# Kernel optimization log

Hardware: AMD Instinct MI355X
Metric: run time of the kernel (lower is better)

The kernel has to match this reference:

```python
import jax, jax.numpy as jnp
import numpy as np

NUM_Q_HEADS = 32
NUM_KV_HEADS = 8
GROUP = NUM_Q_HEADS // NUM_KV_HEADS  # 4, matches hardcoded repeat_interleave(repeats=4)
HEAD_DIM = 128
ROPE_BASE = 10000.0


def _rope_cos_sin(seq_len, head_dim, dtype):
    # [S, D/2] angle tables for rotate-half RoPE
    inv_freq = 1.0 / (ROPE_BASE ** (jnp.arange(0, head_dim, 2, dtype=jnp.float32) / head_dim))
    ang = jnp.arange(seq_len, dtype=jnp.float32)[:, None] * inv_freq[None, :]
    return jnp.cos(ang).astype(dtype), jnp.sin(ang).astype(dtype)


def _apply_rope(x, cos, sin):
    # x: [B, S, H, D]; cos/sin: [S, D/2] broadcast over batch & heads
    x1, x2 = jnp.split(x, 2, axis=-1)
    c = cos[None, :, None, :]
    s = sin[None, :, None, :]
    return jnp.concatenate([x1 * c - x2 * s, x2 * c + x1 * s], axis=-1)


def setup_inputs() -> dict:
    key = jax.random.key(0)
    k1, k2, k3 = jax.random.split(key, 3)
    B, S, E = 2, 2048, 4096
    x = jax.random.normal(k1, (B, S, E), dtype=jnp.float32)
    w_in = jax.random.normal(k2, (6144, E), dtype=jnp.float32) * 0.02   # torch Linear weight [out, in]
    w_out = jax.random.normal(k3, (E, E), dtype=jnp.float32) * 0.02
    return {"x": x, "w_in": w_in, "w_out": w_out}


def reference(x, w_in, w_out):
    B, S, E = x.shape
    D = HEAD_DIM
    qkv = jnp.einsum('bse,fe->bsf', x, w_in)  # [B, S, 6144]
    parts = jnp.split(qkv, GROUP + 2, axis=-1)  # 6 equal chunks of width E//GROUP
    q = jnp.concatenate(parts[:GROUP], axis=-1).reshape(B, S, NUM_Q_HEADS, D)
    k = parts[GROUP].reshape(B, S, NUM_KV_HEADS, D)
    v = parts[GROUP + 1].reshape(B, S, NUM_KV_HEADS, D)

    cos, sin = _rope_cos_sin(S, D, x.dtype)
    q = _apply_rope(q, cos, sin)
    k = _apply_rope(k, cos, sin)

    # GQA without materializing repeated K/V: group q heads by kv head.
    # repeat_interleave(k, 4, dim=2) maps q head h -> kv head h // 4, i.e. q view [B,S,HKV,G,D]
    qg = q.reshape(B, S, NUM_KV_HEADS, GROUP, D)
    scale = 1.0 / jnp.sqrt(jnp.asarray(D, dtype=x.dtype))
    scores = jnp.einsum('bqhgd,bkhd->bhgqk', qg, k) * scale  # [B, HKV, G, S, S]
    causal = jnp.tril(jnp.ones((S, S), dtype=bool))
    scores = jnp.where(causal[None, None, None, :, :], scores, jnp.asarray(-1e30, dtype=scores.dtype))
    probs = jax.nn.softmax(scores, axis=-1)
    out = jnp.einsum('bhgqk,bkhd->bqhgd', probs, v)  # [B, S, HKV, G, D]
    out = out.reshape(B, S, E)
    return jnp.einsum('bse,fe->bsf', out, w_out)
```

## Files before the change

### kernel.cpp

```cpp
#include <hip/hip_runtime.h>
#include <hip/hip_bf16.h>
#include <stdint.h>

typedef unsigned short u16;
typedef __bf16 bf16x8 __attribute__((ext_vector_type(8)));
typedef u16 u16x8 __attribute__((ext_vector_type(8)));
typedef float f32x4 __attribute__((ext_vector_type(4)));

#define DEV __device__ __forceinline__
#define SBAR() asm volatile("s_barrier" ::: "memory")

DEV u16 f2bf(float f) {
  uint32_t u = __builtin_bit_cast(uint32_t, f);
  return (u16)((u + 0x7FFFu + ((u >> 16) & 1u)) >> 16);
}
DEV float bf2f(u16 h) { return __builtin_bit_cast(float, (uint32_t)h << 16); }

DEV void gload_lds16(const void* g, void* l) {
  __builtin_amdgcn_global_load_lds((const __attribute__((address_space(1))) uint32_t*)g,
                                   (__attribute__((address_space(3))) uint32_t*)l, 16, 0, 0);
}

__global__ void cvt_bf16(const float* __restrict__ in, u16* __restrict__ out, int n) {
  int i = (blockIdx.x * 256 + threadIdx.x) * 8;
  if (i >= n) return;
  const float4* p = reinterpret_cast<const float4*>(in + i);
  float4 a = p[0], b = p[1];
  u16x8 o;
  o[0] = f2bf(a.x); o[1] = f2bf(a.y); o[2] = f2bf(a.z); o[3] = f2bf(a.w);
  o[4] = f2bf(b.x); o[5] = f2bf(b.y); o[6] = f2bf(b.z); o[7] = f2bf(b.w);
  *reinterpret_cast<u16x8*>(out + i) = o;
}

__global__ void rope_table(float* __restrict__ ct, float* __restrict__ st) {
  int i = blockIdx.x * 256 + threadIdx.x;
  int s = i >> 6, d = i & 63;
  float invf = powf(10000.0f, -(float)d * (1.0f / 64.0f));
  float ang = (float)s * invf;
  ct[i] = cosf(ang);
  st[i] = sinf(ang);
}

__global__ void rope_apply(u16* __restrict__ qkv, const float* __restrict__ ct, const float* __restrict__ st) {
  int idx = blockIdx.x * 256 + threadIdx.x;
  int grp = idx & 7;
  int head = (idx >> 3) % 40;
  int row = idx / 320;
  int s = row & 2047;
  size_t f0 = head < 32 ? (size_t)head * 128 : (size_t)4096 + (size_t)(head - 32) * 128;
  u16* p = qkv + (size_t)row * 6144 + f0 + grp * 8;
  u16x8 a = *reinterpret_cast<const u16x8*>(p);
  u16x8 b = *reinterpret_cast<const u16x8*>(p + 64);
  const float4* cp = reinterpret_cast<const float4*>(ct + s * 64 + grp * 8);
  const float4* sp = reinterpret_cast<const float4*>(st + s * 64 + grp * 8);
  float4 c0 = cp[0], c1 = cp[1], s0 = sp[0], s1 = sp[1];
  float cc[8] = {c0.x, c0.y, c0.z, c0.w, c1.x, c1.y, c1.z, c1.w};
  float ss[8] = {s0.x, s0.y, s0.z, s0.w, s1.x, s1.y, s1.z, s1.w};
  u16x8 o1, o2;
#pragma unroll
  for (int i = 0; i < 8; i++) {
    float x1 = bf2f(a[i]), x2 = bf2f(b[i]);
    o1[i] = f2bf(x1 * cc[i] - x2 * ss[i]);
    o2[i] = f2bf(x2 * cc[i] + x1 * ss[i]);
  }
  *reinterpret_cast<u16x8*>(p) = o1;
  *reinterpret_cast<u16x8*>(p + 64) = o2;
}

__global__ void prep_vt(const u16* __restrict__ qkv, u16* __restrict__ vtg) {
  int id = blockIdx.x;
  int j = id & 31, kvh = (id >> 5) & 7, b = id >> 8;
  const int tid = threadIdx.x;
  const size_t rowB = (size_t)b * 2048;
  u16* img = vtg + (size_t)id * 8192;
#pragma unroll
  for (int p = 0; p < 4; p++) {
    int lin = p * 256 + tid;
    int d = lin >> 3, c = lin & 7;
    const u16* src = qkv + (rowB + j * 64 + c * 8) * 6144 + 5120 + kvh * 128 + d;
    u16x8 v;
#pragma unroll
    for (int i = 0; i < 8; i++) v[i] = src[(size_t)i * 6144];
    *reinterpret_cast<u16x8*>(img + d * 64 + ((c ^ (d & 7)) << 3)) = v;
  }
}

DEV void store_c(float* C, size_t idx, float v) { C[idx] = v; }
DEV void store_c(u16* C, size_t idx, float v) { C[idx] = f2bf(v); }

template <typename OutT>
__global__ __launch_bounds__(512, 2) void gemm256(const u16* __restrict__ A, const u16* __restrict__ B,
                                                  OutT* __restrict__ C, int M, int N, int K) {
  __shared__ __align__(16) u16 lds[65536];
  char* LB = (char*)lds;
  const int tid = threadIdx.x;
  const int w = tid >> 6, lane = tid & 63;
  const int l15 = lane & 15, l4 = lane >> 4;
  const int wm = w >> 2, wn = w & 3;

  int nwg = gridDim.x;
  int q = nwg >> 3, rr = nwg & 7;
  int xcd = blockIdx.x & 7, idx = blockIdx.x >> 3;
  int sw = (xcd < rr ? xcd * (q + 1) : rr * (q + 1) + (xcd - rr) * q) + idx;
  int gxn = N >> 8;
  int by = sw / gxn, bx = sw - by * gxn;
  const int row0 = by << 8, col0 = bx << 8;
  const int NT = K >> 6;

  const int srow = w * 8 + (lane >> 3);
  const int sc16 = (lane & 7) ^ ((lane >> 3) & 7);
  const u16* gA = A + (size_t)(row0 + srow) * K + sc16 * 8;
  const u16* gB = B + (size_t)(col0 + srow) * K + sc16 * 8;

  const int fl = (l15 & 7) << 4;
  const int aoff = (wm * 128 + l15) * 128 + l4 * 16;
  const int boff = (wn * 64 + l15) * 128 + l4 * 16;

  f32x4 acc[8][4] = {};
  bf16x8 fA[4][2], fB0[2][2], fBc[2][2];

#define STAGE_A(kt, h, base)                                                      \
  {                                                                               \
    const u16* g_ = gA + (size_t)((h)*128) * K + (size_t)(kt)*64;                 \
    gload_lds16(g_, (base) + (h)*16384 + w * 1024);                               \
    gload_lds16(g_ + (size_t)64 * K, (base) + (h)*16384 + 8192 + w * 1024);       \
  }
#define STAGE_B(kt, h, base)                                                      \
  {                                                                               \
    const u16* g_ = gB + (size_t)((h)*128) * K + (size_t)(kt)*64;                 \
    gload_lds16(g_, (base) + (h)*16384 + w * 1024);                               \
    gload_lds16(g_ + (size_t)64 * K, (base) + (h)*16384 + 8192 + w * 1024);       \
  }
#define MFMA_Q(FB, MH, NH)                                                        \
  _Pragma("unroll") for (int kk = 0; kk < 2; kk++) {                              \
    _Pragma("unroll") for (int mf = 0; mf < 4; mf++) {                            \
      _Pragma("unroll") for (int nf = 0; nf < 2; nf++) {                          \
        acc[(MH)*4 + mf][(NH)*2 + nf] = __builtin_amdgcn_mfma_f32_16x16x32_bf16(  \
            fA[mf][kk], FB[nf][kk], acc[(MH)*4 + mf][(NH)*2 + nf], 0, 0, 0);      \
      }                                                                           \
    }                                                                             \
  }

  STAGE_A(0, 0, LB);
  STAGE_A(0, 1, LB);
  STAGE_B(0, 0, LB + 65536);
  STAGE_B(0, 1, LB + 65536);
  STAGE_A(1, 0, LB + 32768);
  STAGE_B(1, 0, LB + 98304);
  STAGE_B(1, 1, LB + 98304);
  asm volatile("s_waitcnt vmcnt(6)" ::: "memory");
  SBAR();

  for (int t = 0; t < NT; ++t) {
    char* ac = LB + (t & 1) * 32768;
    char* bc = LB + 65536 + (t & 1) * 32768;
    char* an = LB + ((t + 1) & 1) * 32768;

#pragma unroll
    for (int mf = 0; mf < 4; mf++)
#pragma unroll
      for (int kk = 0; kk < 2; kk++)
        fA[mf][kk] = *(const bf16x8*)(ac + ((aoff + mf * 2048 + kk * 64) ^ fl));
#pragma unroll
    for (int nf = 0; nf < 2; nf++)
#pragma unroll
      for (int kk = 0; kk < 2; kk++)
        fB0[nf][kk] = *(const bf16x8*)(bc + ((boff + nf * 2048 + kk * 64) ^ fl));
    if (t + 1 < NT) STAGE_A(t + 1, 1, an);
    asm volatile("s_waitcnt lgkmcnt(8)" ::: "memory");
    SBAR();
    asm volatile("s_waitcnt lgkmcnt(0)" ::: "memory");
    __builtin_amdgcn_sched_barrier(0);
    __builtin_amdgcn_s_setprio(1);
    MFMA_Q(fB0, 0, 0);
    __builtin_amdgcn_s_setprio(0);
    SBAR();

#pragma unroll
    for (int nf = 0; nf < 2; nf++)
#pragma unroll
      for (int kk = 0; kk < 2; kk++)
        fBc[nf][kk] = *(const bf16x8*)(bc + ((boff + (nf + 2) * 2048 + kk * 64) ^ fl));
    SBAR();
    asm volatile("s_waitcnt lgkmcnt(0)" ::: "memory");
    __builtin_amdgcn_sched_barrier(0);
    __builtin_amdgcn_s_setprio(1);
    MFMA_Q(fBc, 0, 1);
    __builtin_amdgcn_s_setprio(0);
    SBAR();

#pragma unroll
    for (int mf = 0; mf < 4; mf++)
#pragma unroll
      for (int kk = 0; kk < 2; kk++)
        fA[mf][kk] = *(const bf16x8*)(ac + ((aoff + (mf + 4) * 2048 + kk * 64) ^ fl));
    if (t + 2 < NT) STAGE_B(t + 2, 0, bc);
    SBAR();
    asm volatile("s_waitcnt lgkmcnt(0)" ::: "memory");
    __builtin_amdgcn_sched_barrier(0);
    __builtin_amdgcn_s_setprio(1);
    MFMA_Q(fBc, 1, 1);
    __builtin_amdgcn_s_setprio(0);
    SBAR();

    if (t + 2 < NT) {
      STAGE_A(t + 2, 0, ac);
      STAGE_B(t + 2, 1, bc);
    }
    SBAR();
    __builtin_amdgcn_s_setprio(1);
    MFMA_Q(fB0, 1, 0);
    __builtin_amdgcn_s_setprio(0);
    if (t <= NT - 3) {
      asm volatile("s_waitcnt vmcnt(6)" ::: "memory");
      SBAR();
    } else if (t < NT - 1) {
      asm volatile("s_waitcnt vmcnt(0)" ::: "memory");
      SBAR();
    }
  }

#pragma unroll
  for (int mf = 0; mf < 8; mf++)
#pragma unroll
    for (int nf = 0; nf < 4; nf++)
#pragma unroll
      for (int r = 0; r < 4; r++) {
        size_t row = (size_t)row0 + wm * 128 + mf * 16 + l4 * 4 + r;
        size_t col = (size_t)col0 + wn * 64 + nf * 16 + l15;
        store_c(C, row * (size_t)N + col, acc[mf][nf][r]);
      }
#undef STAGE_A
#undef STAGE_B
#undef MFMA_Q
}

__global__ __launch_bounds__(256, 2) void attn_fwd(const u16* __restrict__ qkv,
                                                   const u16* __restrict__ vtg,
                                                   u16* __restrict__ out) {
  constexpr int S = 2048, F = 6144, E = 4096;
  __shared__ __align__(16) u16 Kt[2 * 8192];
  __shared__ __align__(16) u16 Vt[2 * 8192];
  __shared__ __align__(16) u16 Pl[4 * 2048];

  const int tid = threadIdx.x;
  const int w = tid >> 6, lane = tid & 63;
  const int l15 = lane & 15, l4 = lane >> 4;
  const int pair = blockIdx.x;
  const int b = blockIdx.y >> 5, h = blockIdx.y & 31, kvh = h >> 2;
  const size_t rowB = (size_t)b * S;
  const float sc = 0.08838834764831845f * 1.4426950408889634f;
  const int sgn = tid >> 4, sgc = tid & 15;
  char* PlW = ((char*)Pl) + w * 4096;
  const size_t vtb = (size_t)(b * 8 + kvh) * 32 * 8192;

  auto stage = [&](int j, int buf) {
    char* kd = ((char*)Kt) + buf * 16384 + w * 1024;
    char* vd = ((char*)Vt) + buf * 16384 + w * 1024;
    const u16* vs = vtg + vtb + (size_t)j * 8192 + tid * 8;
#pragma unroll
    for (int p = 0; p < 4; p++) {
      int n = p * 16 + sgn;
      const u16* g = qkv + (rowB + j * 64 + n) * F + 4096 + kvh * 128 + (sgc ^ (n & 7)) * 8;
      gload_lds16(g, kd + p * 4096);
      gload_lds16(vs + p * 2048, vd + p * 4096);
    }
  };

  for (int half = 0; half < 2; ++half) {
    const int t = half ? 15 - pair : pair;
    const int nt = 2 * t + 2;
    const int r0 = t * 128;

    bf16x8 qf[2][4];
    {
      const u16* qp = qkv + (rowB + r0 + w * 32 + l15) * F + h * 128 + l4 * 8;
#pragma unroll
      for (int m = 0; m < 2; m++)
#pragma unroll
        for (int kk = 0; kk < 4; kk++)
          qf[m][kk] = *reinterpret_cast<const bf16x8*>(qp + (size_t)m * 16 * F + kk * 32);
    }

    f32x4 acco[2][8] = {};
    float m_r[2][4], l_r[2][4];
#pragma unroll
    for (int m = 0; m < 2; m++)
#pragma unroll
      for (int r = 0; r < 4; r++) { m_r[m][r] = -1e30f; l_r[m][r] = 0.f; }

    stage(0, 0);
    __syncthreads();

    for (int j = 0; j < nt; ++j) {
      const int cur = j & 1;
      if (j + 1 < nt) stage(j + 1, cur ^ 1);

      const char* kbase = ((const char*)Kt) + cur * 16384;
      f32x4 accs[2][4] = {};
      __builtin_amdgcn_s_setprio(1);
#pragma unroll
      for (int ns = 0; ns < 4; ns++) {
        int n = ns * 16 + l15;
        const char* kb = kbase + n * 256;
#pragma unroll
        for (int kk = 0; kk < 4; kk++) {
          bf16x8 kf = *reinterpret_cast<const bf16x8*>(kb + (((kk * 4 + l4) ^ (n & 7)) << 4));
          accs[0][ns] = __builtin_amdgcn_mfma_f32_16x16x32_bf16(qf[0][kk], kf, accs[0][ns], 0, 0, 0);
          accs[1][ns] = __builtin_amdgcn_mfma_f32_16x16x32_bf16(qf[1][kk], kf, accs[1][ns], 0, 0, 0);
        }
      }
      __builtin_amdgcn_s_setprio(0);

      const int qb = r0 + w * 32 + l4 * 4;
      const int kvb = j * 64 + l15;
      if (j >= 2 * t) {
#pragma unroll
        for (int m = 0; m < 2; m++)
#pragma unroll
          for (int ns = 0; ns < 4; ns++)
#pragma unroll
            for (int r = 0; r < 4; r++)
              accs[m][ns][r] = (kvb + ns * 16 > qb + m * 16 + r) ? -1e30f : accs[m][ns][r] * sc;
      } else {
#pragma unroll
        for (int m = 0; m < 2; m++)
#pragma unroll
          for (int ns = 0; ns < 4; ns++)
#pragma unroll
            for (int r = 0; r < 4; r++) accs[m][ns][r] *= sc;
      }

      float tm[2][4];
#pragma unroll
      for (int m = 0; m < 2; m++)
#pragma unroll
        for (int r = 0; r < 4; r++) {
          float a = fmaxf(fmaxf(accs[m][0][r], accs[m][1][r]), fmaxf(accs[m][2][r], accs[m][3][r]));
          a = fmaxf(a, __shfl_xor(a, 1));
          a = fmaxf(a, __shfl_xor(a, 2));
          a = fmaxf(a, __shfl_xor(a, 4));
          a = fmaxf(a, __shfl_xor(a, 8));
          tm[m][r] = a;
        }
      int needb = 0;
#pragma unroll
      for (int m = 0; m < 2; m++)
#pragma unroll
        for (int r = 0; r < 4; r++) needb |= (tm[m][r] > m_r[m][r] + 8.0f) ? 1 : 0;
      if (__any(needb)) {
#pragma unroll
        for (int m = 0; m < 2; m++)
#pragma unroll
          for (int r = 0; r < 4; r++) {
            float m2 = fmaxf(m_r[m][r], tm[m][r]);
            float fr = exp2f(m_r[m][r] - m2);
            m_r[m][r] = m2;
            l_r[m][r] *= fr;
#pragma unroll
            for (int ns = 0; ns < 8; ns++) acco[m][ns][r] *= fr;
          }
      }
      float ps[2][4] = {};
#pragma unroll
      for (int m = 0; m < 2; m++)
#pragma unroll
        for (int ns = 0; ns < 4; ns++)
#pragma unroll
          for (int r = 0; r < 4; r++) {
            float p = exp2f(accs[m][ns][r] - m_r[m][r]);
            ps[m][r] += p;
            int row = m * 16 + l4 * 4 + r;
            int kv2 = (ns * 16 + l15) * 2;
            *(u16*)(PlW + row * 128 + (kv2 ^ ((row & 7) << 4))) = f2bf(p);
          }
#pragma unroll
      for (int m = 0; m < 2; m++)
#pragma unroll
        for (int r = 0; r < 4; r++) {
          float s2 = ps[m][r];
          s2 += __shfl_xor(s2, 1);
          s2 += __shfl_xor(s2, 2);
          s2 += __shfl_xor(s2, 4);
          s2 += __shfl_xor(s2, 8);
          l_r[m][r] += s2;
        }

      const char* vbase = ((const char*)Vt) + cur * 16384;
      bf16x8 pf[2][2];
#pragma unroll
      for (int m = 0; m < 2; m++)
#pragma unroll
        for (int kk = 0; kk < 2; kk++) {
          int row = m * 16 + l15;
          pf[m][kk] = *reinterpret_cast<const bf16x8*>(PlW + row * 128 + (((kk * 4 + l4) ^ (row & 7)) << 4));
        }
      __builtin_amdgcn_s_setprio(1);
#pragma unroll
      for (int ns = 0; ns < 8; ns++) {
        int d = ns * 16 + l15;
        const char* vb = vbase + d * 128;
#pragma unroll
        for (int kk = 0; kk < 2; kk++) {
          bf16x8 vf = *reinterpret_cast<const bf16x8*>(vb + (((kk * 4 + l4) ^ (d & 7)) << 4));
          acco[0][ns] = __builtin_amdgcn_mfma_f32_16x16x32_bf16(pf[0][kk], vf, acco[0][ns], 0, 0, 0);
          acco[1][ns] = __builtin_amdgcn_mfma_f32_16x16x32_bf16(pf[1][kk], vf, acco[1][ns], 0, 0, 0);
        }
      }
      __builtin_amdgcn_s_setprio(0);

      __syncthreads();
    }

#pragma unroll
    for (int m = 0; m < 2; m++)
#pragma unroll
      for (int r = 0; r < 4; r++) {
        float inv = 1.f / l_r[m][r];
        size_t row = rowB + r0 + w * 32 + m * 16 + l4 * 4 + r;
#pragma unroll
        for (int ns = 0; ns < 8; ns++)
          out[row * E + h * 128 + ns * 16 + l15] = f2bf(acco[m][ns][r] * inv);
      }
  }
}

extern "C" void kernel_launch(void* const* d_in, const int* in_sizes, int n_in,
                              void* d_out, int out_size, void* d_ws, size_t ws_size,
                              hipStream_t stream) {
  const float* x = (const float*)d_in[0];
  const float* w_in = (const float*)d_in[1];
  const float* w_out = (const float*)d_in[2];
  float* out = (float*)d_out;
  char* ws = (char*)d_ws;

  u16* xb = (u16*)(ws);
  u16* wib = (u16*)(ws + 33554432ull);
  u16* wob = (u16*)(ws + 83886080ull);
  u16* qkvb = (u16*)(ws + 117440512ull);
  float* ct = (float*)(ws + 167772160ull);
  float* st = ct + 2048 * 64;
  u16* attnb = xb;
  u16* vtg = wib;

  cvt_bf16<<<8192, 256, 0, stream>>>(x, xb, 16777216);
  cvt_bf16<<<12288, 256, 0, stream>>>(w_in, wib, 25165824);
  cvt_bf16<<<8192, 256, 0, stream>>>(w_out, wob, 16777216);
  rope_table<<<512, 256, 0, stream>>>(ct, st);
  gemm256<u16><<<384, 512, 0, stream>>>(xb, wib, qkvb, 4096, 6144, 4096);
  rope_apply<<<5120, 256, 0, stream>>>(qkvb, ct, st);
  prep_vt<<<512, 256, 0, stream>>>(qkvb, vtg);
  attn_fwd<<<dim3(8, 64), 256, 0, stream>>>(qkvb, vtg, attnb);
  gemm256<float><<<256, 512, 0, stream>>>(attnb, wob, out, 4096, 4096, 4096);
}
```

Baseline: 601.7 us.

## Split QKV projection into full-wave Q GEMM and narrow-tile KV GEMM

The QKV projection is split into two launches. One covers the Q columns with 256x256 tiles (256 workgroups), and a new 256x128-tile kernel covers the K/V columns (256 workgroups). Both write into the strided qkv buffer through an added ldc parameter. The aim is to remove the partial second wave that 384 tiles left on the device, at the cost of lower data reuse per tile in the KV part and an extra launch.

```diff
diff --git a/kernel.cpp b/kernel.cpp
--- a/kernel.cpp
+++ b/kernel.cpp
@@ -90,7 +90,7 @@
 
 template <typename OutT>
 __global__ __launch_bounds__(512, 2) void gemm256(const u16* __restrict__ A, const u16* __restrict__ B,
-                                                  OutT* __restrict__ C, int M, int N, int K) {
+                                                  OutT* __restrict__ C, int M, int N, int K, int ldc) {
   __shared__ __align__(16) u16 lds[65536];
   char* LB = (char*)lds;
   const int tid = threadIdx.x;
@@ -228,11 +228,137 @@
       for (int r = 0; r < 4; r++) {
         size_t row = (size_t)row0 + wm * 128 + mf * 16 + l4 * 4 + r;
         size_t col = (size_t)col0 + wn * 64 + nf * 16 + l15;
-        store_c(C, row * (size_t)N + col, acc[mf][nf][r]);
+        store_c(C, row * (size_t)ldc + col, acc[mf][nf][r]);
       }
 #undef STAGE_A
 #undef STAGE_B
 #undef MFMA_Q
+}
+
+__global__ __launch_bounds__(512, 2) void gemm_bn128(const u16* __restrict__ A, const u16* __restrict__ B,
+                                                     u16* __restrict__ C, int M, int N, int K, int ldc) {
+  __shared__ __align__(16) u16 lds[49152];
+  char* LB = (char*)lds;
+  const int tid = threadIdx.x;
+  const int w = tid >> 6, lane = tid & 63;
+  const int l15 = lane & 15, l4 = lane >> 4;
+  const int wm = w >> 2, wn = w & 3;
+
+  int nwg = gridDim.x;
+  int q = nwg >> 3, rr = nwg & 7;
+  int xcd = blockIdx.x & 7, idx = blockIdx.x >> 3;
+  int sw = (xcd < rr ? xcd * (q + 1) : rr * (q + 1) + (xcd - rr) * q) + idx;
+  int gxn = N >> 7;
+  int by = sw / gxn, bx = sw - by * gxn;
+  const int row0 = by << 8, col0 = bx << 7;
+  const int NT = K >> 6;
+
+  const int srow = w * 8 + (lane >> 3);
+  const int sc16 = (lane & 7) ^ ((lane >> 3) & 7);
+  const u16* gA = A + (size_t)(row0 + srow) * K + sc16 * 8;
+  const u16* gB = B + (size_t)(col0 + srow) * K + sc16 * 8;
+
+  const int fl = (l15 & 7) << 4;
+  const int aoff = (wm * 128 + l15) * 128 + l4 * 16;
+  const int boff = (wn * 32 + l15) * 128 + l4 * 16;
+
+  f32x4 acc[8][2] = {};
+  bf16x8 fA[4][2], fB[2][2];
+
+#define STAGE_A(kt, h, base)                                                      \
+  {                                                                               \
+    const u16* g_ = gA + (size_t)((h)*128) * K + (size_t)(kt)*64;                 \
+    gload_lds16(g_, (base) + (h)*16384 + w * 1024);                               \
+    gload_lds16(g_ + (size_t)64 * K, (base) + (h)*16384 + 8192 + w * 1024);       \
+  }
+#define STAGE_B(kt, base)                                                         \
+  {                                                                               \
+    const u16* g_ = gB + (size_t)(kt)*64;                                         \
+    gload_lds16(g_, (base) + w * 1024);                                           \
+    gload_lds16(g_ + (size_t)64 * K, (base) + 8192 + w * 1024);                   \
+  }
+
+  STAGE_A(0, 0, LB);
+  STAGE_A(0, 1, LB);
+  STAGE_B(0, LB + 65536);
+  STAGE_A(1, 0, LB + 32768);
+  STAGE_B(1, LB + 65536 + 16384);
+  asm volatile("s_waitcnt vmcnt(4)" ::: "memory");
+  SBAR();
+
+  for (int t = 0; t < NT; ++t) {
+    char* ac = LB + (t & 1) * 32768;
+    char* bc = LB + 65536 + (t & 1) * 16384;
+    char* an = LB + ((t + 1) & 1) * 32768;
+
+#pragma unroll
+    for (int mf = 0; mf < 4; mf++)
+#pragma unroll
+      for (int kk = 0; kk < 2; kk++)
+        fA[mf][kk] = *(const bf16x8*)(ac + ((aoff + mf * 2048 + kk * 64) ^ fl));
+#pragma unroll
+    for (int nf = 0; nf < 2; nf++)
+#pragma unroll
+      for (int kk = 0; kk < 2; kk++)
+        fB[nf][kk] = *(const bf16x8*)(bc + ((boff + nf * 2048 + kk * 64) ^ fl));
+    if (t + 1 < NT) STAGE_A(t + 1, 1, an);
+    asm volatile("s_waitcnt lgkmcnt(8)" ::: "memory");
+    SBAR();
+    asm volatile("s_waitcnt lgkmcnt(0)" ::: "memory");
+    __builtin_amdgcn_sched_barrier(0);
+    __builtin_amdgcn_s_setprio(1);
+#pragma unroll
+    for (int kk = 0; kk < 2; kk++)
+#pragma unroll
+      for (int mf = 0; mf < 4; mf++)
+#pragma unroll
+        for (int nf = 0; nf < 2; nf++)
+          acc[mf][nf] = __builtin_amdgcn_mfma_f32_16x16x32_bf16(fA[mf][kk], fB[nf][kk], acc[mf][nf], 0, 0, 0);
+    __builtin_amdgcn_s_setprio(0);
+    SBAR();
+
+#pragma unroll
+    for (int mf = 0; mf < 4; mf++)
+#pragma unroll
+      for (int kk = 0; kk < 2; kk++)
+        fA[mf][kk] = *(const bf16x8*)(ac + ((aoff + (mf + 4) * 2048 + kk * 64) ^ fl));
+    if (t + 2 < NT) {
+      STAGE_A(t + 2, 0, ac);
+      STAGE_B(t + 2, bc);
+    }
+    SBAR();
+    asm volatile("s_waitcnt lgkmcnt(0)" ::: "memory");
+    __builtin_amdgcn_sched_barrier(0);
+    __builtin_amdgcn_s_setprio(1);
+#pragma unroll
+    for (int kk = 0; kk < 2; kk++)
+#pragma unroll
+      for (int mf = 0; mf < 4; mf++)
+#pragma unroll
+        for (int nf = 0; nf < 2; nf++)
+          acc[mf + 4][nf] = __builtin_amdgcn_mfma_f32_16x16x32_bf16(fA[mf][kk], fB[nf][kk], acc[mf + 4][nf], 0, 0, 0);
+    __builtin_amdgcn_s_setprio(0);
+    if (t <= NT - 3) {
+      asm volatile("s_waitcnt vmcnt(4)" ::: "memory");
+      SBAR();
+    } else if (t < NT - 1) {
+      asm volatile("s_waitcnt vmcnt(0)" ::: "memory");
+      SBAR();
+    }
+  }
+
+#pragma unroll
+  for (int mf = 0; mf < 8; mf++)
+#pragma unroll
+    for (int nf = 0; nf < 2; nf++)
+#pragma unroll
+      for (int r = 0; r < 4; r++) {
+        size_t row = (size_t)row0 + wm * 128 + mf * 16 + l4 * 4 + r;
+        size_t col = (size_t)col0 + wn * 32 + nf * 16 + l15;
+        C[row * (size_t)ldc + col] = f2bf(acc[mf][nf][r]);
+      }
+#undef STAGE_A
+#undef STAGE_B
 }
 
 __global__ __launch_bounds__(256, 2) void attn_fwd(const u16* __restrict__ qkv,
@@ -447,9 +573,10 @@
   cvt_bf16<<<12288, 256, 0, stream>>>(w_in, wib, 25165824);
   cvt_bf16<<<8192, 256, 0, stream>>>(w_out, wob, 16777216);
   rope_table<<<512, 256, 0, stream>>>(ct, st);
-  gemm256<u16><<<384, 512, 0, stream>>>(xb, wib, qkvb, 4096, 6144, 4096);
+  gemm256<u16><<<256, 512, 0, stream>>>(xb, wib, qkvb, 4096, 4096, 4096, 6144);
+  gemm_bn128<<<256, 512, 0, stream>>>(xb, wib + (size_t)4096 * 4096, qkvb + 4096, 4096, 2048, 4096, 6144);
   rope_apply<<<5120, 256, 0, stream>>>(qkvb, ct, st);
   prep_vt<<<512, 256, 0, stream>>>(qkvb, vtg);
   attn_fwd<<<dim3(8, 64), 256, 0, stream>>>(qkvb, vtg, attnb);
-  gemm256<float><<<256, 512, 0, stream>>>(attnb, wob, out, 4096, 4096, 4096);
-}
+  gemm256<float><<<256, 512, 0, stream>>>(attnb, wob, out, 4096, 4096, 4096, 4096);
+}
```

Measured after the change: 570.7 us. 1.05x faster.
